# Kernel optimization log

Hardware: AMD Instinct MI355X
Metric: run time of the kernel (lower is better)

The kernel has to match this reference:

```python
import jax, jax.numpy as jnp
import numpy as np

B, NQ, NC, D, H = 4, 4096, 4096, 1024, 16
HD = D // H
LN_EPS = 1e-5


def _layernorm(x, g, b):
    mu = jnp.mean(x, axis=-1, keepdims=True)
    var = jnp.var(x, axis=-1, keepdims=True)
    return (x - mu) * jax.lax.rsqrt(var + LN_EPS) * g + b


def _kernel(x):
    # elu(x) + 1  (strictly positive feature map)
    return jax.nn.elu(x) + 1.0


def setup_inputs() -> dict:
    key = jax.random.key(0)
    ks = jax.random.split(key, 12)
    s = 1.0 / np.sqrt(D)
    return {
        "query": jax.random.normal(ks[0], (B, NQ, D), jnp.float32),
        "context": jax.random.normal(ks[1], (B, NC, D), jnp.float32),
        "q_w": jax.random.uniform(ks[2], (D, D), jnp.float32, -s, s),
        "q_b": jnp.zeros((D,), jnp.float32),
        "k_w": jax.random.uniform(ks[3], (D, D), jnp.float32, -s, s),
        "k_b": jnp.zeros((D,), jnp.float32),
        "v_w": jax.random.uniform(ks[4], (D, D), jnp.float32, -s, s),
        "v_b": jnp.zeros((D,), jnp.float32),
        "o_w": jax.random.uniform(ks[5], (D, D), jnp.float32, -s, s),
        "o_b": jnp.zeros((D,), jnp.float32),
        "lnq_g": jnp.ones((D,), jnp.float32),
        "lnq_b": jnp.zeros((D,), jnp.float32),
        "lnkv_g": jnp.ones((D,), jnp.float32),
        "lnkv_b": jnp.zeros((D,), jnp.float32),
    }


def reference(query, context, q_w, q_b, k_w, k_b, v_w, v_b, o_w, o_b,
              lnq_g, lnq_b, lnkv_g, lnkv_b):
    residual = query
    q = _layernorm(query, lnq_g, lnq_b)
    c = _layernorm(context, lnkv_g, lnkv_b)

    # torch Linear: y = x @ W.T + b ; reshape to (B, H, N, Hd)
    Q = (q @ q_w.T + q_b).reshape(B, NQ, H, HD).transpose(0, 2, 1, 3)
    K = (c @ k_w.T + k_b).reshape(B, NC, H, HD).transpose(0, 2, 1, 3)
    V = (c @ v_w.T + v_b).reshape(B, NC, H, HD).transpose(0, 2, 1, 3)

    Q = _kernel(Q)
    K = _kernel(K)

    # KV: (B, H, Hd, Hd) outer-product accumulation over context length
    KV = jnp.einsum("bhnd,bhne->bhde", K, V)
    K_sum = K.sum(axis=2)                              # (B, H, Hd)
    Z = jnp.einsum("bhqd,bhd->bhq", Q, K_sum)          # (B, H, Nq)
    Z = jnp.maximum(Z, 1e-6)

    out = jnp.einsum("bhqd,bhde->bhqe", Q, KV) / Z[..., None]
    out = out.transpose(0, 2, 1, 3).reshape(B, NQ, D)
    return residual + (out @ o_w.T + o_b)
```

## Files before the change

kernel.cpp:

```cpp
#include <hip/hip_runtime.h>

#define DEV __device__ __forceinline__

typedef __attribute__((ext_vector_type(8))) short short8;
typedef __attribute__((ext_vector_type(4))) short short4v;
typedef __attribute__((ext_vector_type(4))) float f32x4;

DEV float bf2f(unsigned short u) { return __uint_as_float(((unsigned int)u) << 16); }
DEV unsigned short f2bf(float f) {
    unsigned int u = __float_as_uint(f);
    u += 0x7FFFu + ((u >> 16) & 1u);
    return (unsigned short)(u >> 16);
}

DEV void gload_lds16(const void* g, void* l) {
    __builtin_amdgcn_global_load_lds(
        (__attribute__((address_space(1))) unsigned int*)(g),
        (__attribute__((address_space(3))) unsigned int*)(l),
        16, 0, 0);
}

#define NROW 16384
#define DDIM 1024

__global__ __launch_bounds__(256) void ln_kernel(
    const float* __restrict__ query, const float* __restrict__ context,
    const float* __restrict__ lnq_g, const float* __restrict__ lnq_b,
    const float* __restrict__ lnk_g, const float* __restrict__ lnk_b,
    unsigned short* __restrict__ qln, unsigned short* __restrict__ cln)
{
    const int row = blockIdx.x;
    const bool isq = row < NROW;
    const int r = isq ? row : row - NROW;
    const float* src = (isq ? query : context) + (size_t)r * DDIM;
    const float* g   = isq ? lnq_g : lnk_g;
    const float* bb  = isq ? lnq_b : lnk_b;
    unsigned short* dst = (isq ? qln : cln) + (size_t)r * DDIM;

    const int tid = threadIdx.x;
    f32x4 x = *(const f32x4*)(src + tid * 4);
    float s  = x[0] + x[1] + x[2] + x[3];
    float sq = x[0]*x[0] + x[1]*x[1] + x[2]*x[2] + x[3]*x[3];
#pragma unroll
    for (int off = 32; off; off >>= 1) {
        s  += __shfl_xor(s, off);
        sq += __shfl_xor(sq, off);
    }
    __shared__ float red[8];
    const int lane = tid & 63, w = tid >> 6;
    if (lane == 0) { red[w] = s; red[4 + w] = sq; }
    __syncthreads();
    s  = red[0] + red[1] + red[2] + red[3];
    sq = red[4] + red[5] + red[6] + red[7];
    const float mu  = s * (1.0f / DDIM);
    const float var = sq * (1.0f / DDIM) - mu * mu;
    const float rstd = rsqrtf(var + 1e-5f);

    f32x4 gv = *(const f32x4*)(g + tid * 4);
    f32x4 bv = *(const f32x4*)(bb + tid * 4);
    short4v o;
#pragma unroll
    for (int j = 0; j < 4; ++j)
        o[j] = (short)f2bf((x[j] - mu) * rstd * gv[j] + bv[j]);
    *(short4v*)(dst + tid * 4) = o;
}

__global__ __launch_bounds__(256) void conv_w(
    const float* __restrict__ a, const float* __restrict__ b,
    const float* __restrict__ c, const float* __restrict__ d,
    unsigned short* __restrict__ out)
{
    const int i = blockIdx.x * 256 + threadIdx.x;
    const int mat = i >> 18;
    const int idx = (i & 262143) * 4;
    const float* src = mat == 0 ? a : mat == 1 ? b : mat == 2 ? c : d;
    f32x4 v = *(const f32x4*)(src + idx);
    short4v o;
#pragma unroll
    for (int j = 0; j < 4; ++j) o[j] = (short)f2bf(v[j]);
    *(short4v*)(out + (size_t)mat * 1048576 + idx) = o;
}

template <int MODE>
__global__ __launch_bounds__(512, 2) void gemm_bt(
    const unsigned short* __restrict__ A, const unsigned short* __restrict__ Bm,
    void* __restrict__ Cout, const float* __restrict__ bias,
    const float* __restrict__ resid, int ldc)
{
    __shared__ __attribute__((aligned(16))) unsigned short sA[2][16384];
    __shared__ __attribute__((aligned(16))) unsigned short sB[2][16384];

    const int bid = blockIdx.x;
    const int l = (bid & 7) * 32 + (bid >> 3);
    int m0, n0;
    if (MODE == 0 || MODE == 3) { m0 = (l >> 2) * 256; n0 = (l & 3) * 256; }
    else                        { m0 = (l & 3) * 256;  n0 = (l >> 2) * 256; }

    const int tid = threadIdx.x;
    const int lane = tid & 63, w = tid >> 6;
    const int wr = w >> 2, wc = w & 3;
    const int lr = lane & 15, lg = lane >> 4;

    const int srow = tid >> 3;
    const int cswz = (tid & 7) ^ (srow & 7);
    const unsigned short* gA0 = A  + (size_t)(m0 + srow) * 1024 + cswz * 8;
    const unsigned short* gB0 = Bm + (size_t)(n0 + srow) * 1024 + cswz * 8;

    const int sw0 = ((0 + lg) ^ (lr & 7)) * 8;
    const int sw1 = ((4 + lg) ^ (lr & 7)) * 8;

    f32x4 acc[8][4];
#pragma unroll
    for (int i = 0; i < 8; ++i)
#pragma unroll
        for (int j = 0; j < 4; ++j)
#pragma unroll
            for (int e = 0; e < 4; ++e) acc[i][j][e] = 0.0f;

#define STAGE(T, BUF)                                                        \
    {                                                                        \
        const unsigned short* ga = gA0 + (T) * 64;                           \
        const unsigned short* gb = gB0 + (T) * 64;                           \
        unsigned short* da = &sA[BUF][0] + tid * 8;                          \
        unsigned short* db = &sB[BUF][0] + tid * 8;                          \
        _Pragma("unroll")                                                    \
        for (int L = 0; L < 4; ++L)                                          \
            gload_lds16(ga + (size_t)L * 65536, da + L * 4096);              \
        _Pragma("unroll")                                                    \
        for (int L = 0; L < 4; ++L)                                          \
            gload_lds16(gb + (size_t)L * 65536, db + L * 4096);              \
    }

    STAGE(0, 0);
    STAGE(1, 1);
    asm volatile("s_waitcnt vmcnt(8)" ::: "memory");
    __builtin_amdgcn_s_barrier();

    for (int t = 0; t < 16; ++t) {
        const unsigned short* bufA = &sA[t & 1][0];
        const unsigned short* bufB = &sB[t & 1][0];

        short8 af[8][2], bv[4][2];
#pragma unroll
        for (int mt = 0; mt < 8; ++mt) {
            const int ra = (wr * 128 + mt * 16 + lr) * 64;
            af[mt][0] = *(const short8*)&bufA[ra + sw0];
            af[mt][1] = *(const short8*)&bufA[ra + sw1];
        }
#pragma unroll
        for (int nt = 0; nt < 4; ++nt) {
            const int rb = (wc * 64 + nt * 16 + lr) * 64;
            bv[nt][0] = *(const short8*)&bufB[rb + sw0];
            bv[nt][1] = *(const short8*)&bufB[rb + sw1];
        }
        asm volatile("s_waitcnt lgkmcnt(0)" ::: "memory");
        __builtin_amdgcn_s_barrier();

        if (t + 2 < 16) STAGE(t + 2, t & 1);

        __builtin_amdgcn_s_setprio(1);
#pragma unroll
        for (int kk = 0; kk < 2; ++kk)
#pragma unroll
            for (int mt = 0; mt < 8; ++mt)
#pragma unroll
                for (int nt = 0; nt < 4; ++nt)
                    acc[mt][nt] = __builtin_amdgcn_mfma_f32_16x16x32_bf16(
                        af[mt][kk], bv[nt][kk], acc[mt][nt], 0, 0, 0);
        __builtin_amdgcn_s_setprio(0);

        if (t + 2 < 16) asm volatile("s_waitcnt vmcnt(8)" ::: "memory");
        else            asm volatile("s_waitcnt vmcnt(0)" ::: "memory");
        __builtin_amdgcn_s_barrier();
    }
#undef STAGE

#pragma unroll
    for (int mt = 0; mt < 8; ++mt) {
#pragma unroll
        for (int nt = 0; nt < 4; ++nt) {
            const int col = n0 + wc * 64 + nt * 16 + lr;
#pragma unroll
            for (int i = 0; i < 4; ++i) {
                const int row = m0 + wr * 128 + mt * 16 + lg * 4 + i;
                float v = acc[mt][nt][i];
                if (MODE == 0) { v += bias[col]; v = v > 0.0f ? v + 1.0f : __expf(v); }
                if (MODE == 1) { v += bias[row]; v = v > 0.0f ? v + 1.0f : __expf(v); }
                if (MODE == 2) { v += bias[row]; }
                if (MODE == 3) { v += bias[col] + resid[(size_t)row * 1024 + col]; }
                if (MODE == 3)
                    ((float*)Cout)[(size_t)row * 1024 + col] = v;
                else
                    ((unsigned short*)Cout)[(size_t)row * (size_t)ldc + col] = f2bf(v);
            }
        }
    }
}

__global__ __launch_bounds__(256) void kv_kernel(
    const unsigned short* __restrict__ VT, const unsigned short* __restrict__ KT,
    float* __restrict__ KVTp)
{
    const int bh = blockIdx.x, sp = blockIdx.y;
    const int b = bh >> 4, h = bh & 15;
    const int tid = threadIdx.x, lane = tid & 63, w = tid >> 6;
    const int lr = lane & 15, lg = lane >> 4;

    f32x4 acc[4][4];
#pragma unroll
    for (int i = 0; i < 4; ++i)
#pragma unroll
        for (int j = 0; j < 4; ++j)
#pragma unroll
            for (int e = 0; e < 4; ++e) acc[i][j][e] = 0.0f;

    const size_t colbase = (size_t)b * 4096 + sp * 1024 + w * 256 + lg * 8;
    const unsigned short* va = VT + (size_t)(h * 64 + lr) * NROW + colbase;
    const unsigned short* ka = KT + (size_t)(h * 64 + lr) * NROW + colbase;

    for (int ks = 0; ks < 8; ++ks) {
        short8 af[4], bfv[4];
#pragma unroll
        for (int mt = 0; mt < 4; ++mt)
            af[mt] = *(const short8*)(va + (size_t)mt * 16 * NROW + ks * 32);
#pragma unroll
        for (int nt = 0; nt < 4; ++nt)
            bfv[nt] = *(const short8*)(ka + (size_t)nt * 16 * NROW + ks * 32);
#pragma unroll
        for (int mt = 0; mt < 4; ++mt)
#pragma unroll
            for (int nt = 0; nt < 4; ++nt)
                acc[mt][nt] = __builtin_amdgcn_mfma_f32_16x16x32_bf16(
                    af[mt], bfv[nt], acc[mt][nt], 0, 0, 0);
    }

    __shared__ float red4[4][4096];
#pragma unroll
    for (int mt = 0; mt < 4; ++mt)
#pragma unroll
        for (int nt = 0; nt < 4; ++nt)
#pragma unroll
            for (int i = 0; i < 4; ++i)
                red4[w][(mt * 16 + lg * 4 + i) * 64 + nt * 16 + lr] = acc[mt][nt][i];
    __syncthreads();
    float* out = KVTp + ((size_t)sp * 64 + bh) * 4096;
    for (int i = tid; i < 4096; i += 256)
        out[i] = red4[0][i] + red4[1][i] + red4[2][i] + red4[3][i];
}

__global__ __launch_bounds__(256) void ksum_kernel(
    const unsigned short* __restrict__ KT, float* __restrict__ Ksum)
{
    const int bh = blockIdx.x, quad = blockIdx.y;
    const int b = bh >> 4, h = bh & 15;
    const int tid = threadIdx.x, lane = tid & 63, w = tid >> 6;
    const int dbase = quad * 16 + w * 4;
#pragma unroll
    for (int dd = 0; dd < 4; ++dd) {
        const int d = dbase + dd;
        const unsigned short* p = KT + (size_t)(h * 64 + d) * NROW + b * 4096 + lane * 8;
        float s = 0.0f;
#pragma unroll
        for (int it = 0; it < 8; ++it) {
            short8 v = *(const short8*)(p + it * 512);
#pragma unroll
            for (int j = 0; j < 8; ++j) s += bf2f((unsigned short)v[j]);
        }
#pragma unroll
        for (int off = 32; off; off >>= 1) s += __shfl_xor(s, off);
        if (lane == 0) Ksum[bh * 64 + d] = s;
    }
}

__global__ __launch_bounds__(256) void z_kernel(
    const unsigned short* __restrict__ Q, const float* __restrict__ Ksum,
    float* __restrict__ invZ)
{
    const int gid = blockIdx.x * 256 + threadIdx.x;
    const int n = gid >> 4, h = gid & 15;
    const int b = n >> 12;
    const unsigned short* q = Q + (size_t)n * DDIM + h * 64;
    const float* ks = Ksum + ((b << 4) + h) * 64;
    float z = 0.0f;
#pragma unroll
    for (int it = 0; it < 8; ++it) {
        short8 v = *(const short8*)(q + it * 8);
#pragma unroll
        for (int j = 0; j < 8; ++j) z += bf2f((unsigned short)v[j]) * ks[it * 8 + j];
    }
    invZ[gid] = 1.0f / fmaxf(z, 1e-6f);
}

__global__ __launch_bounds__(256) void a2_kernel(
    const unsigned short* __restrict__ Q, const float* __restrict__ KVTp,
    const float* __restrict__ invZ, unsigned short* __restrict__ A2)
{
    const int m0 = blockIdx.x * 128, h = blockIdx.y;
    const int b = m0 >> 12, bh = (b << 4) + h;
    const int tid = threadIdx.x, lane = tid & 63, w = tid >> 6;
    const int wr = w >> 1, wc = w & 1;
    const int lr = lane & 15, lg = lane >> 4;

    f32x4 acc[4][2];
#pragma unroll
    for (int i = 0; i < 4; ++i)
#pragma unroll
        for (int j = 0; j < 2; ++j)
#pragma unroll
            for (int e = 0; e < 4; ++e) acc[i][j][e] = 0.0f;

    const unsigned short* qa = Q + (size_t)(m0 + wr * 64 + lr) * DDIM + h * 64 + lg * 8;
    const float* kvb = KVTp + (size_t)bh * 4096 + (wc * 32 + lr) * 64 + lg * 8;

#pragma unroll
    for (int ks = 0; ks < 2; ++ks) {
        short8 af[4];
#pragma unroll
        for (int mt = 0; mt < 4; ++mt)
            af[mt] = *(const short8*)(qa + (size_t)mt * 16 * DDIM + ks * 32);
        short8 bfv[2];
#pragma unroll
        for (int nt = 0; nt < 2; ++nt) {
            const float* p = kvb + nt * 16 * 64 + ks * 32;
            short8 t;
#pragma unroll
            for (int j = 0; j < 8; ++j) {
                float v = p[j] + p[j + 262144] + p[j + 2 * 262144] + p[j + 3 * 262144];
                t[j] = (short)f2bf(v);
            }
            bfv[nt] = t;
        }
#pragma unroll
        for (int mt = 0; mt < 4; ++mt)
#pragma unroll
            for (int nt = 0; nt < 2; ++nt)
                acc[mt][nt] = __builtin_amdgcn_mfma_f32_16x16x32_bf16(
                    af[mt], bfv[nt], acc[mt][nt], 0, 0, 0);
    }

#pragma unroll
    for (int mt = 0; mt < 4; ++mt)
#pragma unroll
        for (int nt = 0; nt < 2; ++nt)
#pragma unroll
            for (int i = 0; i < 4; ++i) {
                const int row = m0 + wr * 64 + mt * 16 + lg * 4 + i;
                const int col = h * 64 + wc * 32 + nt * 16 + lr;
                const float v = acc[mt][nt][i] * invZ[row * 16 + h];
                A2[(size_t)row * DDIM + col] = f2bf(v);
            }
}

extern "C" void kernel_launch(void* const* d_in, const int* in_sizes, int n_in,
                              void* d_out, int out_size, void* d_ws, size_t ws_size,
                              hipStream_t stream)
{
    const float* query   = (const float*)d_in[0];
    const float* context = (const float*)d_in[1];
    const float* q_w = (const float*)d_in[2];
    const float* q_b = (const float*)d_in[3];
    const float* k_w = (const float*)d_in[4];
    const float* k_b = (const float*)d_in[5];
    const float* v_w = (const float*)d_in[6];
    const float* v_b = (const float*)d_in[7];
    const float* o_w = (const float*)d_in[8];
    const float* o_b = (const float*)d_in[9];
    const float* lnq_g = (const float*)d_in[10];
    const float* lnq_b = (const float*)d_in[11];
    const float* lnk_g = (const float*)d_in[12];
    const float* lnk_b = (const float*)d_in[13];

    char* ws = (char*)d_ws;
    unsigned short* WQ  = (unsigned short*)(ws);
    unsigned short* WK  = (unsigned short*)(ws + (2u << 20));
    unsigned short* WV  = (unsigned short*)(ws + (4u << 20));
    unsigned short* WO  = (unsigned short*)(ws + (6u << 20));
    unsigned short* QLN = (unsigned short*)(ws + (8u << 20));
    unsigned short* CLN = (unsigned short*)(ws + (40u << 20));
    unsigned short* Qm  = (unsigned short*)(ws + (72u << 20));
    unsigned short* KT  = (unsigned short*)(ws + (104u << 20));
    unsigned short* VT  = (unsigned short*)(ws + (136u << 20));
    float* KVTp = (float*)(ws + (168u << 20));
    float* Ksum = (float*)(ws + (172u << 20));
    float* invZ = (float*)(ws + (173u << 20));
    unsigned short* A2 = QLN;

    conv_w<<<4096, 256, 0, stream>>>(q_w, k_w, v_w, o_w, WQ);
    ln_kernel<<<2 * NROW, 256, 0, stream>>>(query, context, lnq_g, lnq_b,
                                            lnk_g, lnk_b, QLN, CLN);
    gemm_bt<0><<<256, 512, 0, stream>>>(QLN, WQ, Qm, q_b, nullptr, 1024);
    gemm_bt<1><<<256, 512, 0, stream>>>(WK, CLN, KT, k_b, nullptr, NROW);
    gemm_bt<2><<<256, 512, 0, stream>>>(WV, CLN, VT, v_b, nullptr, NROW);
    kv_kernel<<<dim3(64, 4), 256, 0, stream>>>(VT, KT, KVTp);
    ksum_kernel<<<dim3(64, 4), 256, 0, stream>>>(KT, Ksum);
    z_kernel<<<1024, 256, 0, stream>>>(Qm, Ksum, invZ);
    a2_kernel<<<dim3(128, 16), 256, 0, stream>>>(Qm, KVTp, invZ, A2);
    gemm_bt<3><<<256, 512, 0, stream>>>(A2, WO, d_out, o_b, query, 1024);
}
```

Measured before the change: 288.3 us.

## Split GEMM K-step into four quadrant phases interleaving LDS reads with MFMA

Restructures the GEMM main loop into four sub-phases, each computing one quadrant of the 8x4 accumulator tile. LDS fragment loads for the next quadrant and the global-to-LDS prefetch for B and then A are interleaved between the MFMA groups, with a barrier between phases. The aim is to hide LDS read latency and spread global prefetch issue across the compute instead of loading all fragments up front. The cost is more barriers per iteration and a more delicate ordering of waitcnt and prefetch buffer reuse.

After: 277.5 us. -3.7%, faster.

```diff
diff --git a/kernel.cpp b/kernel.cpp
--- a/kernel.cpp
+++ b/kernel.cpp
@@ -87,8 +87,9 @@
     void* __restrict__ Cout, const float* __restrict__ bias,
     const float* __restrict__ resid, int ldc)
 {
-    __shared__ __attribute__((aligned(16))) unsigned short sA[2][16384];
-    __shared__ __attribute__((aligned(16))) unsigned short sB[2][16384];
+    __shared__ __attribute__((aligned(16))) unsigned short smem[65536];
+    unsigned short* sAb = smem;
+    unsigned short* sBb = smem + 32768;
 
     const int bid = blockIdx.x;
     const int l = (bid & 7) * 32 + (bid >> 3);
@@ -117,63 +118,102 @@
 #pragma unroll
             for (int e = 0; e < 4; ++e) acc[i][j][e] = 0.0f;
 
-#define STAGE(T, BUF)                                                        \
-    {                                                                        \
-        const unsigned short* ga = gA0 + (T) * 64;                           \
-        const unsigned short* gb = gB0 + (T) * 64;                           \
-        unsigned short* da = &sA[BUF][0] + tid * 8;                          \
-        unsigned short* db = &sB[BUF][0] + tid * 8;                          \
-        _Pragma("unroll")                                                    \
-        for (int L = 0; L < 4; ++L)                                          \
-            gload_lds16(ga + (size_t)L * 65536, da + L * 4096);              \
-        _Pragma("unroll")                                                    \
-        for (int L = 0; L < 4; ++L)                                          \
-            gload_lds16(gb + (size_t)L * 65536, db + L * 4096);              \
-    }
-
-    STAGE(0, 0);
-    STAGE(1, 1);
-    asm volatile("s_waitcnt vmcnt(8)" ::: "memory");
-    __builtin_amdgcn_s_barrier();
+#define STG(GP, SP, T)                                                        \
+    {                                                                         \
+        const unsigned short* g = (GP) + (T) * 64;                            \
+        unsigned short* d = (SP) + ((T) & 1) * 16384 + tid * 8;               \
+        _Pragma("unroll")                                                     \
+        for (int L = 0; L < 4; ++L)                                           \
+            gload_lds16(g + (size_t)L * 65536, d + L * 4096);                 \
+    }
+
+    STG(gB0, sBb, 0); STG(gA0, sAb, 0); STG(gB0, sBb, 1); STG(gA0, sAb, 1);
 
     for (int t = 0; t < 16; ++t) {
-        const unsigned short* bufA = &sA[t & 1][0];
-        const unsigned short* bufB = &sB[t & 1][0];
-
-        short8 af[8][2], bv[4][2];
-#pragma unroll
-        for (int mt = 0; mt < 8; ++mt) {
+        const unsigned short* bA = sAb + (t & 1) * 16384;
+        const unsigned short* bB = sBb + (t & 1) * 16384;
+        short8 afl[4][2], afh[4][2], bvl[2][2], bvh[2][2];
+
+        if (t == 15) asm volatile("s_waitcnt vmcnt(0)" ::: "memory");
+        else         asm volatile("s_waitcnt vmcnt(8)" ::: "memory");
+        __builtin_amdgcn_s_barrier();
+#pragma unroll
+        for (int mt = 0; mt < 4; ++mt) {
             const int ra = (wr * 128 + mt * 16 + lr) * 64;
-            af[mt][0] = *(const short8*)&bufA[ra + sw0];
-            af[mt][1] = *(const short8*)&bufA[ra + sw1];
-        }
-#pragma unroll
-        for (int nt = 0; nt < 4; ++nt) {
+            afl[mt][0] = *(const short8*)&bA[ra + sw0];
+            afl[mt][1] = *(const short8*)&bA[ra + sw1];
+        }
+#pragma unroll
+        for (int nt = 0; nt < 2; ++nt) {
             const int rb = (wc * 64 + nt * 16 + lr) * 64;
-            bv[nt][0] = *(const short8*)&bufB[rb + sw0];
-            bv[nt][1] = *(const short8*)&bufB[rb + sw1];
-        }
+            bvl[nt][0] = *(const short8*)&bB[rb + sw0];
+            bvl[nt][1] = *(const short8*)&bB[rb + sw1];
+        }
+        __builtin_amdgcn_s_setprio(1);
+#pragma unroll
+        for (int kk = 0; kk < 2; ++kk)
+#pragma unroll
+            for (int mt = 0; mt < 4; ++mt)
+#pragma unroll
+                for (int nt = 0; nt < 2; ++nt)
+                    acc[mt][nt] = __builtin_amdgcn_mfma_f32_16x16x32_bf16(
+                        afl[mt][kk], bvl[nt][kk], acc[mt][nt], 0, 0, 0);
+        __builtin_amdgcn_s_setprio(0);
         asm volatile("s_waitcnt lgkmcnt(0)" ::: "memory");
         __builtin_amdgcn_s_barrier();
 
-        if (t + 2 < 16) STAGE(t + 2, t & 1);
-
+#pragma unroll
+        for (int nt = 0; nt < 2; ++nt) {
+            const int rb = (wc * 64 + (nt + 2) * 16 + lr) * 64;
+            bvh[nt][0] = *(const short8*)&bB[rb + sw0];
+            bvh[nt][1] = *(const short8*)&bB[rb + sw1];
+        }
         __builtin_amdgcn_s_setprio(1);
 #pragma unroll
         for (int kk = 0; kk < 2; ++kk)
 #pragma unroll
-            for (int mt = 0; mt < 8; ++mt)
-#pragma unroll
-                for (int nt = 0; nt < 4; ++nt)
-                    acc[mt][nt] = __builtin_amdgcn_mfma_f32_16x16x32_bf16(
-                        af[mt][kk], bv[nt][kk], acc[mt][nt], 0, 0, 0);
+            for (int mt = 0; mt < 4; ++mt)
+#pragma unroll
+                for (int nt = 0; nt < 2; ++nt)
+                    acc[mt][nt + 2] = __builtin_amdgcn_mfma_f32_16x16x32_bf16(
+                        afl[mt][kk], bvh[nt][kk], acc[mt][nt + 2], 0, 0, 0);
         __builtin_amdgcn_s_setprio(0);
-
-        if (t + 2 < 16) asm volatile("s_waitcnt vmcnt(8)" ::: "memory");
-        else            asm volatile("s_waitcnt vmcnt(0)" ::: "memory");
+        asm volatile("s_waitcnt lgkmcnt(0)" ::: "memory");
         __builtin_amdgcn_s_barrier();
-    }
-#undef STAGE
+
+#pragma unroll
+        for (int mt = 0; mt < 4; ++mt) {
+            const int ra = (wr * 128 + (mt + 4) * 16 + lr) * 64;
+            afh[mt][0] = *(const short8*)&bA[ra + sw0];
+            afh[mt][1] = *(const short8*)&bA[ra + sw1];
+        }
+        if (t + 2 < 16) STG(gB0, sBb, t + 2);
+        __builtin_amdgcn_s_setprio(1);
+#pragma unroll
+        for (int kk = 0; kk < 2; ++kk)
+#pragma unroll
+            for (int mt = 0; mt < 4; ++mt)
+#pragma unroll
+                for (int nt = 0; nt < 2; ++nt)
+                    acc[mt + 4][nt + 2] = __builtin_amdgcn_mfma_f32_16x16x32_bf16(
+                        afh[mt][kk], bvh[nt][kk], acc[mt + 4][nt + 2], 0, 0, 0);
+        __builtin_amdgcn_s_setprio(0);
+        asm volatile("s_waitcnt lgkmcnt(0)" ::: "memory");
+        __builtin_amdgcn_s_barrier();
+
+        if (t + 2 < 16) STG(gA0, sAb, t + 2);
+        __builtin_amdgcn_s_setprio(1);
+#pragma unroll
+        for (int kk = 0; kk < 2; ++kk)
+#pragma unroll
+            for (int mt = 0; mt < 4; ++mt)
+#pragma unroll
+                for (int nt = 0; nt < 2; ++nt)
+                    acc[mt + 4][nt] = __builtin_amdgcn_mfma_f32_16x16x32_bf16(
+                        afh[mt][kk], bvl[nt][kk], acc[mt + 4][nt], 0, 0, 0);
+        __builtin_amdgcn_s_setprio(0);
+    }
+#undef STG
 
 #pragma unroll
     for (int mt = 0; mt < 8; ++mt) {
```
